# Optimization experiments

Hardware: AMD Instinct MI355X
Metric: run time of the kernel (lower is better)

The kernel has to match this reference:

```python
import jax, jax.numpy as jnp
import numpy as np

N_USERS = 200_000
N_ITEMS = 100_000
EMB = 64
N_EDGES = 5_000_000
N_LAYERS = 3


def setup_inputs() -> dict:
    key = jax.random.key(0)
    k1, k2, k3, k4, k5 = jax.random.split(key, 5)
    emb_user = jax.random.normal(k1, (N_USERS, EMB), dtype=jnp.float32) * 0.1
    emb_item = jax.random.normal(k2, (N_ITEMS, EMB), dtype=jnp.float32) * 0.1
    n_nodes = N_USERS + N_ITEMS
    edge_row = jax.random.randint(k3, (N_EDGES,), 0, n_nodes, dtype=jnp.int32)
    edge_col = jax.random.randint(k4, (N_EDGES,), 0, n_nodes, dtype=jnp.int32)
    # normalized adjacency values (positive, < 1), stand-in for D^-1/2 A D^-1/2
    edge_val = jax.random.uniform(k5, (N_EDGES,), dtype=jnp.float32)
    return {"emb_user": emb_user, "emb_item": emb_item,
            "edge_val": edge_val, "edge_row": edge_row, "edge_col": edge_col}


def reference(emb_user, emb_item, edge_val, edge_row, edge_col):
    n_users = emb_user.shape[0]
    n_nodes = n_users + emb_item.shape[0]
    # 0th-layer embedding matrix: cat(user, item)  [N, D]
    x = jnp.concatenate([emb_user, emb_item], axis=0)
    layers = [x]
    for _ in range(N_LAYERS):
        # SpMM: out[r] += val * x[c] for each edge (r, c)
        x = jax.ops.segment_sum(edge_val[:, None] * x[edge_col], edge_row,
                                num_segments=n_nodes)
        layers.append(x)
    # layer combination: mean over all layers
    agg = jnp.mean(jnp.stack(layers, axis=0), axis=0)
    return agg[:n_users], agg[n_users:]
```

## Files before the change

kernel.cpp:

```cpp
#include <hip/hip_runtime.h>

#define N_USERS 200000
#define N_ITEMS 100000
#define N_NODES 300000
#define EMB     64
#define N_EDGES 5000000

typedef float f32x4 __attribute__((ext_vector_type(4)));
typedef _Float16 f16;
typedef f16 f16x4 __attribute__((ext_vector_type(4)));

struct alignas(8) SRec { unsigned int rc; float val; };

#define BSHIFT 8
#define BROWS  (1 << BSHIFT)
#define NBUCK  ((N_NODES + BROWS - 1) >> BSHIFT)
#define CAP    5120
#define BIN_CHUNK 16384
#define COLMASK 0x7FFFFu
#define INIT_BLOCKS 2048

__global__ __launch_bounds__(256) void fused_init_bin_kernel(
    const float* __restrict__ user, const float* __restrict__ item,
    f16* __restrict__ x0,
    const int4* __restrict__ row4, const int4* __restrict__ col4,
    const float4* __restrict__ val4,
    int* __restrict__ bcursor, SRec* __restrict__ stage, int bin_blocks)
{
    int t = threadIdx.x;
    if ((int)blockIdx.x < bin_blocks) {
        __shared__ int hist[NBUCK];
        __shared__ int base_[NBUCK];
        const int Q = N_EDGES / 4;
        long q0 = (long)blockIdx.x * (BIN_CHUNK / 4);

        for (int k = t; k < NBUCK; k += 256) hist[k] = 0;
        __syncthreads();

        int4 ra[16];
        const bool full = (q0 + (BIN_CHUNK / 4) <= Q);
        if (full) {
            #pragma unroll
            for (int k = 0; k < 16; ++k)
                ra[k] = row4[q0 + k * 256 + t];
            #pragma unroll
            for (int k = 0; k < 16; ++k) {
                atomicAdd(&hist[ra[k].x >> BSHIFT], 1);
                atomicAdd(&hist[ra[k].y >> BSHIFT], 1);
                atomicAdd(&hist[ra[k].z >> BSHIFT], 1);
                atomicAdd(&hist[ra[k].w >> BSHIFT], 1);
            }
        } else {
            #pragma unroll
            for (int k = 0; k < 16; ++k) {
                long q = q0 + k * 256 + t;
                if (q < Q) {
                    ra[k] = row4[q];
                    atomicAdd(&hist[ra[k].x >> BSHIFT], 1);
                    atomicAdd(&hist[ra[k].y >> BSHIFT], 1);
                    atomicAdd(&hist[ra[k].z >> BSHIFT], 1);
                    atomicAdd(&hist[ra[k].w >> BSHIFT], 1);
                }
            }
        }
        __syncthreads();
        for (int k = t; k < NBUCK; k += 256) {
            int h = hist[k];
            base_[k] = h ? atomicAdd(&bcursor[k], h) : 0;
            hist[k] = 0;
        }
        __syncthreads();
        #pragma unroll
        for (int g = 0; g < 4; ++g) {
            int4 c4[4]; float4 v4[4];
            #pragma unroll
            for (int j = 0; j < 4; ++j) {
                long q = q0 + (g * 4 + j) * 256 + t;
                if (q < Q) { c4[j] = col4[q]; v4[j] = val4[q]; }
            }
            #pragma unroll
            for (int j = 0; j < 4; ++j) {
                long q = q0 + (g * 4 + j) * 256 + t;
                if (q < Q) {
                    int4 r = ra[g * 4 + j];
                    int   rr[4] = {r.x, r.y, r.z, r.w};
                    int   cc[4] = {c4[j].x, c4[j].y, c4[j].z, c4[j].w};
                    float vv[4] = {v4[j].x, v4[j].y, v4[j].z, v4[j].w};
                    #pragma unroll
                    for (int m = 0; m < 4; ++m) {
                        int b   = rr[m] >> BSHIFT;
                        int pos = base_[b] + atomicAdd(&hist[b], 1);
                        SRec s;
                        s.rc  = ((unsigned)(rr[m] & (BROWS - 1)) << 19)
                              | (unsigned)cc[m];
                        s.val = vv[m];
                        stage[(size_t)b * CAP + pos] = s;
                    }
                }
            }
        }
    } else {
        const int nu4 = N_USERS * EMB / 4;
        const int nt4 = N_NODES * EMB / 4;
        int i0 = ((int)blockIdx.x - bin_blocks) * 256 + t;
        const int stride = INIT_BLOCKS * 256;
        for (int i = i0; i < nt4; i += stride) {
            float4 vv = (i < nu4) ? reinterpret_cast<const float4*>(user)[i]
                                  : reinterpret_cast<const float4*>(item)[i - nu4];
            f16x4 hx = {(f16)vv.x, (f16)vv.y, (f16)vv.z, (f16)vv.w};
            reinterpret_cast<f16x4*>(x0)[i] = hx;
        }
    }
}

__global__ __launch_bounds__(256) void bucket_scan_scatter_kernel(
    const SRec* __restrict__ stage, const int* __restrict__ bsize,
    int* __restrict__ start, unsigned short* __restrict__ cnt16,
    int* __restrict__ pcol, f16* __restrict__ pval)
{
    __shared__ int cur[BROWS];
    __shared__ int sc[256];
    __shared__ int lcol[CAP];
    __shared__ f16 lval[CAP];

    int b    = blockIdx.x;
    int t    = threadIdx.x;
    int row0 = b << BSHIFT;
    int rows = N_NODES - row0; if (rows > BROWS) rows = BROWS;

    const int  size = bsize[b];
    const int  base = b * CAP;
    const SRec* seg = stage + (size_t)b * CAP;

    cur[t] = 0;
    __syncthreads();

    for (int e = t; e < size; e += 256)
        atomicAdd(&cur[seg[e].rc >> 19], 1);
    __syncthreads();

    int a = cur[t];
    sc[t] = a;
    __syncthreads();
    for (int ofs = 1; ofs < 256; ofs <<= 1) {
        int v = (t >= ofs) ? sc[t - ofs] : 0;
        __syncthreads();
        sc[t] += v;
        __syncthreads();
    }
    int excl = sc[t] - a;
    cur[t] = excl;
    if (t < rows) {
        start[row0 + t] = base + excl;
        cnt16[row0 + t] = (unsigned short)a;
    }
    __syncthreads();

    for (int e = t; e < size; e += 256) {
        SRec srec = seg[e];
        int idx = atomicAdd(&cur[srec.rc >> 19], 1);
        lcol[idx] = (int)(srec.rc & COLMASK);
        lval[idx] = (f16)srec.val;
    }
    __syncthreads();

    for (int i = t; i < size; i += 256) pcol[base + i] = lcol[i];
    for (int i = t; i < size; i += 256) pval[base + i] = lval[i];
}

__global__ __launch_bounds__(256, 4) void spmm_csr_kernel(
    const f16* __restrict__ x, const int* __restrict__ pcol,
    const f16* __restrict__ pval, const int* __restrict__ start,
    const unsigned short* __restrict__ cnt16,
    f16* __restrict__ y,
    const f16* __restrict__ xa, const f16* __restrict__ xb,
    float* __restrict__ out, int mode)
{
    int g = blockIdx.x * (256 / 16) + (threadIdx.x >> 4);
    if (g >= N_NODES) return;
    const int lane16 = threadIdx.x & 15;
    const int d      = lane16 * 4;
    const int gbase  = threadIdx.x & 48;

    int beg = start[g];
    int end = beg + cnt16[g];
    float4 acc = {0.f, 0.f, 0.f, 0.f};

    for (int jb = beg; jb < end; jb += 16) {
        int   mycol = 0; float myval = 0.f;
        if (jb + lane16 < end) {
            mycol = pcol[jb + lane16];
            myval = (float)pval[jb + lane16];
        }

        int   cols[16];
        float vals[16];
        #pragma unroll
        for (int k = 0; k < 16; ++k) {
            cols[k] = __shfl(mycol, gbase + k, 64);
            vals[k] = __shfl(myval, gbase + k, 64);
        }

        f16x4 xv[16];
        #pragma unroll
        for (int k = 0; k < 16; ++k) {
            xv[k] = *reinterpret_cast<const f16x4*>(
                x + (size_t)cols[k] * EMB + d);
        }

        #pragma unroll
        for (int k = 0; k < 16; ++k) {
            acc.x += vals[k] * (float)xv[k].x;
            acc.y += vals[k] * (float)xv[k].y;
            acc.z += vals[k] * (float)xv[k].z;
            acc.w += vals[k] * (float)xv[k].w;
        }
    }

    const size_t rofs = (size_t)g * EMB + d;
    if (mode == 0) {
        f16x4 hy = {(f16)acc.x, (f16)acc.y, (f16)acc.z, (f16)acc.w};
        *reinterpret_cast<f16x4*>(y + rofs) = hy;
    } else {
        f16x4 v0 = *reinterpret_cast<const f16x4*>(xa + rofs);
        f16x4 v1 = *reinterpret_cast<const f16x4*>(xb + rofs);
        f16x4 v2 = *reinterpret_cast<const f16x4*>(x  + rofs);
        f32x4 o;
        o.x = 0.25f * ((float)v0.x + (float)v1.x + (float)v2.x + acc.x);
        o.y = 0.25f * ((float)v0.y + (float)v1.y + (float)v2.y + acc.y);
        o.z = 0.25f * ((float)v0.z + (float)v1.z + (float)v2.z + acc.z);
        o.w = 0.25f * ((float)v0.w + (float)v1.w + (float)v2.w + acc.w);
        __builtin_nontemporal_store(o, reinterpret_cast<f32x4*>(out + rofs));
    }
}

__global__ __launch_bounds__(256) void init_kernel(
    const float* __restrict__ user, const float* __restrict__ item,
    float* __restrict__ x, float* __restrict__ out)
{
    const int nu4 = N_USERS * EMB / 4;
    const int nt4 = N_NODES * EMB / 4;
    int i = blockIdx.x * blockDim.x + threadIdx.x;
    if (i >= nt4) return;
    float4 v = (i < nu4) ? reinterpret_cast<const float4*>(user)[i]
                         : reinterpret_cast<const float4*>(item)[i - nu4];
    reinterpret_cast<float4*>(x)[i]   = v;
    reinterpret_cast<float4*>(out)[i] = v;
}

__global__ __launch_bounds__(256) void spmm_atomic_kernel(
    const float* __restrict__ x, const float* __restrict__ val,
    const int* __restrict__ row, const int* __restrict__ col,
    float* __restrict__ y)
{
    int t = blockIdx.x * blockDim.x + threadIdx.x;
    int e = t >> 4;
    if (e >= N_EDGES) return;
    int d = (t & 15) * 4;
    int   r = row[e];
    int   c = col[e];
    float v = val[e];
    float4 xv = *reinterpret_cast<const float4*>(x + c * EMB + d);
    float* yp = y + r * EMB + d;
    unsafeAtomicAdd(yp + 0, v * xv.x);
    unsafeAtomicAdd(yp + 1, v * xv.y);
    unsafeAtomicAdd(yp + 2, v * xv.z);
    unsafeAtomicAdd(yp + 3, v * xv.w);
}

__global__ __launch_bounds__(256) void addscale_kernel(
    const float* __restrict__ xl, float* __restrict__ out, float scale)
{
    const int nt4 = N_NODES * EMB / 4;
    int i = blockIdx.x * blockDim.x + threadIdx.x;
    if (i >= nt4) return;
    float4 a = reinterpret_cast<float4*>(out)[i];
    float4 b = reinterpret_cast<const float4*>(xl)[i];
    a.x = (a.x + b.x) * scale;
    a.y = (a.y + b.y) * scale;
    a.z = (a.z + b.z) * scale;
    a.w = (a.w + b.w) * scale;
    reinterpret_cast<float4*>(out)[i] = a;
}

extern "C" void kernel_launch(void* const* d_in, const int* in_sizes, int n_in,
                              void* d_out, int out_size, void* d_ws, size_t ws_size,
                              hipStream_t stream) {
    const float* emb_user = (const float*)d_in[0];
    const float* emb_item = (const float*)d_in[1];
    const float* edge_val = (const float*)d_in[2];
    const int*   edge_row = (const int*)d_in[3];
    const int*   edge_col = (const int*)d_in[4];
    float* out = (float*)d_out;

    const size_t node_elems = (size_t)N_NODES * EMB;
    char* ws = (char*)d_ws;

    const size_t off_bufA    = 0;
    const size_t off_bufB    = off_bufA + node_elems * sizeof(float);
    const size_t off_pcol    = off_bufB + node_elems * sizeof(float);
    const size_t off_pval    = off_pcol + (size_t)NBUCK * CAP * sizeof(int);
    const size_t off_start   = off_pval + (size_t)NBUCK * CAP * sizeof(f16);
    const size_t off_cnt16   = off_start + (N_NODES + 4) * sizeof(int);
    const size_t off_bcursor = off_cnt16 + (N_NODES + 4) * sizeof(unsigned short);
    const size_t needed      = off_bcursor + (NBUCK + 4) * sizeof(int);

    const int nt4       = N_NODES * EMB / 4;
    const int el_blocks = (nt4 + 255) / 256;
    const int e_blocks  = (N_EDGES + 255) / 256;

    static_assert((size_t)NBUCK * CAP * sizeof(SRec) <= (size_t)N_NODES * EMB * sizeof(float),
                  "stage must fit in bufB region");

    if (ws_size >= needed) {
        f16*  x0buf   = (f16*) (ws + off_bufA);
        f16*  x2buf   = (f16*) (ws + off_bufA) + node_elems;
        f16*  x1buf   = (f16*) (ws + off_bufB);
        int*  pcol    = (int*) (ws + off_pcol);
        f16*  pval    = (f16*) (ws + off_pval);
        int*  start   = (int*) (ws + off_start);
        unsigned short* cnt16 = (unsigned short*)(ws + off_cnt16);
        int*  bcursor = (int*) (ws + off_bcursor);
        SRec* stage   = (SRec*)(ws + off_bufB);

        hipMemsetAsync(bcursor, 0, (NBUCK + 4) * sizeof(int), stream);

        const int bin_blocks = (N_EDGES + BIN_CHUNK - 1) / BIN_CHUNK;
        fused_init_bin_kernel<<<bin_blocks + INIT_BLOCKS, 256, 0, stream>>>(
            emb_user, emb_item, x0buf,
            (const int4*)edge_row, (const int4*)edge_col, (const float4*)edge_val,
            bcursor, stage, bin_blocks);

        bucket_scan_scatter_kernel<<<NBUCK, 256, 0, stream>>>(
            stage, bcursor, start, cnt16, pcol, pval);

        const int row_blocks = (N_NODES + 15) / 16;
        spmm_csr_kernel<<<row_blocks, 256, 0, stream>>>(
            x0buf, pcol, pval, start, cnt16, x1buf, nullptr, nullptr, nullptr, 0);
        spmm_csr_kernel<<<row_blocks, 256, 0, stream>>>(
            x1buf, pcol, pval, start, cnt16, x2buf, nullptr, nullptr, nullptr, 0);
        spmm_csr_kernel<<<row_blocks, 256, 0, stream>>>(
            x2buf, pcol, pval, start, cnt16, nullptr, x0buf, x1buf, out, 1);
    } else {
        float* fbufA = (float*)(ws + off_bufA);
        float* fbufB = (float*)(ws + off_bufB);
        init_kernel<<<el_blocks, 256, 0, stream>>>(emb_user, emb_item, fbufA, out);
        const int ew_blocks = (N_EDGES * 16 + 255) / 256;
        float* cur = fbufA;
        float* nxt = fbufB;
        for (int layer = 0; layer < 3; ++layer) {
            hipMemsetAsync(nxt, 0, node_elems * sizeof(float), stream);
            spmm_atomic_kernel<<<ew_blocks, 256, 0, stream>>>(
                cur, edge_val, edge_row, edge_col, nxt);
            addscale_kernel<<<el_blocks, 256, 0, stream>>>(
                nxt, out, (layer == 2) ? 0.25f : 1.0f);
            float* tmp = cur; cur = nxt; nxt = tmp;
        }
    }
}
```

Baseline: 569.5 us.

## Widen row buckets to 1024 rows and use 1024-thread bin/scatter blocks

Grows the bucket size from 256 to 1024 rows, which cuts the bucket count fourfold and raises per-bucket capacity to 20000. The binning and bucket scan/scatter kernels now run 1024 threads per block, and the per-thread edge preload drops from 16 to 4 int4s. The aim is fewer, larger buckets, so there is less global atomic cursor traffic and better occupancy per block. In exchange, the scatter kernel now needs about 120KB of LDS per block, which limits how many blocks fit on a CU. Bucket overflow is also a risk, since a 1024-row bucket averages about 17000 edges against a cap of 20000.

```diff
diff --git a/kernel.cpp b/kernel.cpp
--- a/kernel.cpp
+++ b/kernel.cpp
@@ -12,15 +12,16 @@
 
 struct alignas(8) SRec { unsigned int rc; float val; };
 
-#define BSHIFT 8
+#define BSHIFT 10
 #define BROWS  (1 << BSHIFT)
 #define NBUCK  ((N_NODES + BROWS - 1) >> BSHIFT)
-#define CAP    5120
+#define CAP    20000
 #define BIN_CHUNK 16384
+#define BIN_THREADS 1024
 #define COLMASK 0x7FFFFu
-#define INIT_BLOCKS 2048
-
-__global__ __launch_bounds__(256) void fused_init_bin_kernel(
+#define INIT_BLOCKS 512
+
+__global__ __launch_bounds__(1024) void fused_init_bin_kernel(
     const float* __restrict__ user, const float* __restrict__ item,
     f16* __restrict__ x0,
     const int4* __restrict__ row4, const int4* __restrict__ col4,
@@ -34,17 +35,17 @@
         const int Q = N_EDGES / 4;
         long q0 = (long)blockIdx.x * (BIN_CHUNK / 4);
 
-        for (int k = t; k < NBUCK; k += 256) hist[k] = 0;
-        __syncthreads();
-
-        int4 ra[16];
+        for (int k = t; k < NBUCK; k += BIN_THREADS) hist[k] = 0;
+        __syncthreads();
+
+        int4 ra[4];
         const bool full = (q0 + (BIN_CHUNK / 4) <= Q);
         if (full) {
             #pragma unroll
-            for (int k = 0; k < 16; ++k)
-                ra[k] = row4[q0 + k * 256 + t];
-            #pragma unroll
-            for (int k = 0; k < 16; ++k) {
+            for (int k = 0; k < 4; ++k)
+                ra[k] = row4[q0 + k * BIN_THREADS + t];
+            #pragma unroll
+            for (int k = 0; k < 4; ++k) {
                 atomicAdd(&hist[ra[k].x >> BSHIFT], 1);
                 atomicAdd(&hist[ra[k].y >> BSHIFT], 1);
                 atomicAdd(&hist[ra[k].z >> BSHIFT], 1);
@@ -52,8 +53,8 @@
             }
         } else {
             #pragma unroll
-            for (int k = 0; k < 16; ++k) {
-                long q = q0 + k * 256 + t;
+            for (int k = 0; k < 4; ++k) {
+                long q = q0 + k * BIN_THREADS + t;
                 if (q < Q) {
                     ra[k] = row4[q];
                     atomicAdd(&hist[ra[k].x >> BSHIFT], 1);
@@ -64,46 +65,50 @@
             }
         }
         __syncthreads();
-        for (int k = t; k < NBUCK; k += 256) {
+        for (int k = t; k < NBUCK; k += BIN_THREADS) {
             int h = hist[k];
             base_[k] = h ? atomicAdd(&bcursor[k], h) : 0;
             hist[k] = 0;
         }
         __syncthreads();
+        int4 c4[4]; float4 v4[4];
+        if (full) {
+            #pragma unroll
+            for (int k = 0; k < 4; ++k) {
+                c4[k] = col4[q0 + k * BIN_THREADS + t];
+                v4[k] = val4[q0 + k * BIN_THREADS + t];
+            }
+        } else {
+            #pragma unroll
+            for (int k = 0; k < 4; ++k) {
+                long q = q0 + k * BIN_THREADS + t;
+                if (q < Q) { c4[k] = col4[q]; v4[k] = val4[q]; }
+            }
+        }
         #pragma unroll
-        for (int g = 0; g < 4; ++g) {
-            int4 c4[4]; float4 v4[4];
-            #pragma unroll
-            for (int j = 0; j < 4; ++j) {
-                long q = q0 + (g * 4 + j) * 256 + t;
-                if (q < Q) { c4[j] = col4[q]; v4[j] = val4[q]; }
-            }
-            #pragma unroll
-            for (int j = 0; j < 4; ++j) {
-                long q = q0 + (g * 4 + j) * 256 + t;
-                if (q < Q) {
-                    int4 r = ra[g * 4 + j];
-                    int   rr[4] = {r.x, r.y, r.z, r.w};
-                    int   cc[4] = {c4[j].x, c4[j].y, c4[j].z, c4[j].w};
-                    float vv[4] = {v4[j].x, v4[j].y, v4[j].z, v4[j].w};
-                    #pragma unroll
-                    for (int m = 0; m < 4; ++m) {
-                        int b   = rr[m] >> BSHIFT;
-                        int pos = base_[b] + atomicAdd(&hist[b], 1);
-                        SRec s;
-                        s.rc  = ((unsigned)(rr[m] & (BROWS - 1)) << 19)
-                              | (unsigned)cc[m];
-                        s.val = vv[m];
-                        stage[(size_t)b * CAP + pos] = s;
-                    }
+        for (int k = 0; k < 4; ++k) {
+            long q = q0 + k * BIN_THREADS + t;
+            if (full || q < Q) {
+                int   rr[4] = {ra[k].x, ra[k].y, ra[k].z, ra[k].w};
+                int   cc[4] = {c4[k].x, c4[k].y, c4[k].z, c4[k].w};
+                float vv[4] = {v4[k].x, v4[k].y, v4[k].z, v4[k].w};
+                #pragma unroll
+                for (int m = 0; m < 4; ++m) {
+                    int b   = rr[m] >> BSHIFT;
+                    int pos = base_[b] + atomicAdd(&hist[b], 1);
+                    SRec s;
+                    s.rc  = ((unsigned)(rr[m] & (BROWS - 1)) << 19)
+                          | (unsigned)cc[m];
+                    s.val = vv[m];
+                    stage[(size_t)b * CAP + pos] = s;
                 }
             }
         }
     } else {
         const int nu4 = N_USERS * EMB / 4;
         const int nt4 = N_NODES * EMB / 4;
-        int i0 = ((int)blockIdx.x - bin_blocks) * 256 + t;
-        const int stride = INIT_BLOCKS * 256;
+        int i0 = ((int)blockIdx.x - bin_blocks) * BIN_THREADS + t;
+        const int stride = INIT_BLOCKS * BIN_THREADS;
         for (int i = i0; i < nt4; i += stride) {
             float4 vv = (i < nu4) ? reinterpret_cast<const float4*>(user)[i]
                                   : reinterpret_cast<const float4*>(item)[i - nu4];
@@ -113,13 +118,13 @@
     }
 }
 
-__global__ __launch_bounds__(256) void bucket_scan_scatter_kernel(
+__global__ __launch_bounds__(1024) void bucket_scan_scatter_kernel(
     const SRec* __restrict__ stage, const int* __restrict__ bsize,
     int* __restrict__ start, unsigned short* __restrict__ cnt16,
     int* __restrict__ pcol, f16* __restrict__ pval)
 {
     __shared__ int cur[BROWS];
-    __shared__ int sc[256];
+    __shared__ int sc[1024];
     __shared__ int lcol[CAP];
     __shared__ f16 lval[CAP];
 
@@ -135,14 +140,14 @@
     cur[t] = 0;
     __syncthreads();
 
-    for (int e = t; e < size; e += 256)
+    for (int e = t; e < size; e += 1024)
         atomicAdd(&cur[seg[e].rc >> 19], 1);
     __syncthreads();
 
     int a = cur[t];
     sc[t] = a;
     __syncthreads();
-    for (int ofs = 1; ofs < 256; ofs <<= 1) {
+    for (int ofs = 1; ofs < 1024; ofs <<= 1) {
         int v = (t >= ofs) ? sc[t - ofs] : 0;
         __syncthreads();
         sc[t] += v;
@@ -156,7 +161,7 @@
     }
     __syncthreads();
 
-    for (int e = t; e < size; e += 256) {
+    for (int e = t; e < size; e += 1024) {
         SRec srec = seg[e];
         int idx = atomicAdd(&cur[srec.rc >> 19], 1);
         lcol[idx] = (int)(srec.rc & COLMASK);
@@ -164,8 +169,8 @@
     }
     __syncthreads();
 
-    for (int i = t; i < size; i += 256) pcol[base + i] = lcol[i];
-    for (int i = t; i < size; i += 256) pval[base + i] = lval[i];
+    for (int i = t; i < size; i += 1024) pcol[base + i] = lcol[i];
+    for (int i = t; i < size; i += 1024) pval[base + i] = lval[i];
 }
 
 __global__ __launch_bounds__(256, 4) void spmm_csr_kernel(
@@ -326,12 +331,12 @@
         hipMemsetAsync(bcursor, 0, (NBUCK + 4) * sizeof(int), stream);
 
         const int bin_blocks = (N_EDGES + BIN_CHUNK - 1) / BIN_CHUNK;
-        fused_init_bin_kernel<<<bin_blocks + INIT_BLOCKS, 256, 0, stream>>>(
+        fused_init_bin_kernel<<<bin_blocks + INIT_BLOCKS, BIN_THREADS, 0, stream>>>(
             emb_user, emb_item, x0buf,
             (const int4*)edge_row, (const int4*)edge_col, (const float4*)edge_val,
             bcursor, stage, bin_blocks);
 
-        bucket_scan_scatter_kernel<<<NBUCK, 256, 0, stream>>>(
+        bucket_scan_scatter_kernel<<<NBUCK, 1024, 0, stream>>>(
             stage, bcursor, start, cnt16, pcol, pval);
 
         const int row_blocks = (N_NODES + 15) / 16;
```

After: 549.6 us. 1.04x faster.
